# Optimization experiments

Hardware: AMD Instinct MI355X
Metric: run time of the kernel (lower is better)

The kernel has to match this reference:

```python
import jax, jax.numpy as jnp
import numpy as np
from functools import partial

D_MODEL = 768
N_LAYER = 2
VOCAB = 50264  # 50257 padded to multiple of 8
D_STATE = 16
D_INNER = 2 * D_MODEL
DT_RANK = 48
D_CONV = 4
EPS = 1e-5
ZOH_EPS = 1e-7
B, L = 2, 1024


def setup_inputs() -> dict:
    key = jax.random.key(0)
    ks = jax.random.split(key, 16)
    s = 0.02
    inp = {
        'input_ids': jax.random.randint(ks[0], (B, L), 0, VOCAB, dtype=jnp.int32),
        'embedding': jax.random.normal(ks[1], (VOCAB, D_MODEL), jnp.float32) * s,
        'in_w': jax.random.normal(ks[2], (N_LAYER, D_MODEL, 2 * D_INNER), jnp.float32) * s,
        'in_b': jnp.zeros((N_LAYER, 2 * D_INNER), jnp.float32),
        'conv_w': jax.random.normal(ks[3], (N_LAYER, D_INNER, D_CONV), jnp.float32) * s,
        'conv_b': jnp.zeros((N_LAYER, D_INNER), jnp.float32),
        'xproj_w': jax.random.normal(ks[4], (N_LAYER, D_INNER, DT_RANK + 2 * D_STATE), jnp.float32) * s,
        'dt_w': jax.random.normal(ks[5], (N_LAYER, DT_RANK, D_INNER), jnp.float32) * s,
        'dt_b': jnp.zeros((N_LAYER, D_INNER), jnp.float32),
        'A_log': jnp.broadcast_to(jnp.log(jnp.arange(1, D_STATE + 1, dtype=jnp.float32))[None, None, :], (N_LAYER, D_INNER, D_STATE)).copy(),
        'Dp': jnp.ones((N_LAYER, D_INNER), jnp.float32),
        'out_w': jax.random.normal(ks[6], (N_LAYER, D_INNER, D_MODEL), jnp.float32) * s,
        'out_b': jnp.zeros((N_LAYER, D_MODEL), jnp.float32),
        'norm_w': jnp.ones((N_LAYER, D_MODEL), jnp.float32),
        'normf_w': jnp.ones((D_MODEL,), jnp.float32),
    }
    return inp


def rmsnorm(x, w):
    return x * jax.lax.rsqrt(jnp.mean(x * x, axis=-1, keepdims=True) + EPS) * w


def mamba_block(x, in_w, in_b, conv_w, conv_b, xproj_w, dt_w, dt_b, A_log, Dp, out_w, out_b):
    # x: (b, l, d_model)
    xr = x @ in_w + in_b                       # (b, l, 2*d_inner)
    xi, res = jnp.split(xr, 2, axis=-1)        # each (b, l, d_inner)
    # causal depthwise conv1d (torch pads d_conv-1 both sides then truncates to l)
    xc = jnp.transpose(xi, (0, 2, 1))          # (b, d_inner, l)
    xc = jax.lax.conv_general_dilated(
        xc, conv_w[:, None, :], (1,), [(D_CONV - 1, 0)],
        dimension_numbers=('NCH', 'OIH', 'NCH'), feature_group_count=D_INNER)
    xc = xc + conv_b[None, :, None]
    u = jax.nn.silu(jnp.transpose(xc, (0, 2, 1)))  # (b, l, d_inner)
    res = jax.nn.silu(res)
    # generate time-varying SSM params
    dbc = u @ xproj_w                          # (b, l, dt_rank + 2n)
    dt, Bm, Cm = jnp.split(dbc, [DT_RANK, DT_RANK + D_STATE], axis=-1)
    delta = jax.nn.softplus(dt @ dt_w + dt_b)  # (b, l, d_inner)
    A = -jnp.exp(A_log)                        # (d_inner, n)
    # ZOH discretization
    dA = jnp.exp(jnp.einsum('bld,dn->bldn', delta, A))            # (b,l,d_in,n)
    zoh = (dA - 1.0) / (A + ZOH_EPS)                               # (b,l,d_in,n)
    dBu = zoh * Bm[:, :, None, :] * u[..., None]                   # (b,l,d_in,n)
    # selective scan over l
    def step(s, inputs):
        dA_t, dBu_t, C_t = inputs              # (b,d_in,n),(b,d_in,n),(b,n)
        s = dA_t * s + dBu_t
        y = jnp.einsum('bdn,bn->bd', s, C_t)
        return s, y
    s0 = jnp.zeros((u.shape[0], D_INNER, D_STATE), u.dtype)
    _, ys = jax.lax.scan(step, s0, (jnp.moveaxis(dA, 1, 0), jnp.moveaxis(dBu, 1, 0), jnp.moveaxis(Cm, 1, 0)))
    y = jnp.moveaxis(ys, 0, 1) + u * Dp        # (b, l, d_inner)
    y = y * res
    return y @ out_w + out_b


def forward(input_ids, embedding, in_w, in_b, conv_w, conv_b, xproj_w, dt_w, dt_b, A_log, Dp, out_w, out_b, norm_w, normf_w):
    x = embedding[input_ids]                   # (b, l, d_model)
    for i in range(N_LAYER):
        mixed = mamba_block(x, in_w[i], in_b[i], conv_w[i], conv_b[i], xproj_w[i],
                            dt_w[i], dt_b[i], A_log[i], Dp[i], out_w[i], out_b[i])
        x = rmsnorm(mixed + x, norm_w[i])      # ResidualBlock: norm(mixer(x)+x)
    x = rmsnorm(x, normf_w)
    return x @ embedding.T                     # tied lm_head, (b, l, vocab)


def reference(input_ids, embedding, in_w, in_b, conv_w, conv_b, xproj_w, dt_w, dt_b, A_log, Dp, out_w, out_b, norm_w, normf_w):
    return forward(input_ids, embedding, in_w, in_b, conv_w, conv_b, xproj_w,
                   dt_w, dt_b, A_log, Dp, out_w, out_b, norm_w, normf_w)
```

## Files before the change

### kernel.cpp

```cpp
#include <hip/hip_runtime.h>
#include <math.h>
#include <stdint.h>

#define BB 2
#define LL 1024
#define DM 768
#define NL 2
#define VV 50264
#define VPAD 50304
#define DS 16
#define DI 1536
#define DR 48
#define DC 4
#define MM (BB*LL)

#define CH 32
#define NC (LL/CH)
#define CONVL 16

#define KS 8

#define TS 64
#define KT 16

typedef __attribute__((ext_vector_type(8))) short short8;
typedef __attribute__((ext_vector_type(4))) float f32x4;

#define AS3(p) ((__attribute__((address_space(3))) unsigned int*)(unsigned int)(uintptr_t)(p))
#define AS1(p) ((const __attribute__((address_space(1))) unsigned int*)(uintptr_t)(p))

__device__ __forceinline__ unsigned short f2bf(float v) {
    union { float f; unsigned u; } x; x.f = v;
    unsigned r = x.u + 0x7fffu + ((x.u >> 16) & 1u);
    return (unsigned short)(r >> 16);
}
__device__ __forceinline__ float bf2f(unsigned short h) {
    union { unsigned u; float f; } x; x.u = (unsigned)h << 16;
    return x.f;
}

__global__ __launch_bounds__(256) void embed_kernel(
    const int* __restrict__ ids, const float* __restrict__ emb,
    float* __restrict__ x, unsigned short* __restrict__ x16)
{
    int m = blockIdx.x;
    int v = ids[m];
    const float* src = emb + (size_t)v * DM;
    float* dst = x + (size_t)m * DM;
    unsigned short* dst16 = x16 + (size_t)m * DM;
    for (int i = threadIdx.x; i < DM; i += 256) {
        float f = src[i];
        dst[i] = f;
        dst16[i] = f2bf(f);
    }
}

__global__ __launch_bounds__(256) void emb_convert_kernel(
    const float* __restrict__ emb, unsigned short* __restrict__ out)
{
    size_t i8 = (size_t)blockIdx.x * 256 + threadIdx.x;
    size_t row = i8 / 96;
    size_t col8 = (i8 - row * 96) * 8;
    if (row >= VPAD) return;
    ushort4 o0, o1;
    if (row < VV) {
        const float* p = emb + row * DM + col8;
        float4 v0 = *(const float4*)p;
        float4 v1 = *(const float4*)(p + 4);
        o0.x = f2bf(v0.x); o0.y = f2bf(v0.y); o0.z = f2bf(v0.z); o0.w = f2bf(v0.w);
        o1.x = f2bf(v1.x); o1.y = f2bf(v1.y); o1.z = f2bf(v1.z); o1.w = f2bf(v1.w);
    } else {
        o0 = make_ushort4(0, 0, 0, 0);
        o1 = o0;
    }
    unsigned short* op = out + row * DM + col8;
    *(ushort4*)op = o0;
    *(ushort4*)(op + 4) = o1;
}

__global__ __launch_bounds__(256) void transpose_bf16_kernel(
    const float* __restrict__ in, unsigned short* __restrict__ out, int R, int C)
{
    __shared__ float t[32][33];
    int l = blockIdx.z;
    int r0 = blockIdx.y * 32, c0 = blockIdx.x * 32;
    int tx = threadIdx.x & 31, ty = threadIdx.x >> 5;
    const float* ip = in + (size_t)l * R * C;
    unsigned short* op = out + (size_t)l * C * R;
    #pragma unroll
    for (int j = 0; j < 32; j += 8)
        t[ty + j][tx] = ip[(size_t)(r0 + ty + j) * C + c0 + tx];
    __syncthreads();
    #pragma unroll
    for (int j = 0; j < 32; j += 8)
        op[(size_t)(c0 + ty + j) * R + r0 + tx] = f2bf(t[tx][ty + j]);
}

__global__ __launch_bounds__(256) void gemm_mfma_bt(
    const unsigned short* __restrict__ A, const unsigned short* __restrict__ B,
    const float* __restrict__ bias, unsigned short* __restrict__ C16,
    int M, int N, int K, int MT, int NTILES)
{
    int T = MT * NTILES;
    int q = T >> 3, r = T & 7;
    int orig = blockIdx.x;
    int xcd = orig & 7, u = orig >> 3;
    int wg = (xcd < r ? xcd * (q + 1) : r * (q + 1) + (xcd - r) * q) + u;
    int mt = wg % MT, nt = wg / MT;

    __shared__ unsigned short As[3][128 * 32];
    __shared__ unsigned short Bs[3][128 * 32];
    int tid = threadIdx.x;
    int w = tid >> 6, lane = tid & 63;
    int m0 = mt * 128, n0 = nt * 128;

    int rA = lane >> 2;
    int kb = (lane & 3) * 8;
    const unsigned short* gA0 = A + (size_t)(m0 + w * 16 + rA) * K + kb;
    const unsigned short* gA1 = gA0 + (size_t)64 * K;
    const unsigned short* gB0 = B + (size_t)(n0 + w * 16 + rA) * K + kb;
    const unsigned short* gB1 = gB0 + (size_t)64 * K;

    int lr = lane & 15, lk = lane >> 4;
    int wr = (w >> 1) * 64, wc = (w & 1) * 64;

    f32x4 acc[4][4] = {};

#define STAGE(k0, buf) do { \
    __builtin_amdgcn_global_load_lds(AS1(gA0 + (k0)), AS3(&As[buf][(w * 16) * 32]), 16, 0, 0); \
    __builtin_amdgcn_global_load_lds(AS1(gA1 + (k0)), AS3(&As[buf][(64 + w * 16) * 32]), 16, 0, 0); \
    __builtin_amdgcn_global_load_lds(AS1(gB0 + (k0)), AS3(&Bs[buf][(w * 16) * 32]), 16, 0, 0); \
    __builtin_amdgcn_global_load_lds(AS1(gB1 + (k0)), AS3(&Bs[buf][(64 + w * 16) * 32]), 16, 0, 0); \
} while (0)

#define COMPUTE(buf) do { \
    short8 a[4], b[4]; \
    _Pragma("unroll") \
    for (int f = 0; f < 4; ++f) \
        a[f] = *(const short8*)&As[buf][(wr + f * 16 + lr) * 32 + lk * 8]; \
    _Pragma("unroll") \
    for (int f = 0; f < 4; ++f) \
        b[f] = *(const short8*)&Bs[buf][(wc + f * 16 + lr) * 32 + lk * 8]; \
    _Pragma("unroll") \
    for (int i = 0; i < 4; ++i) \
        _Pragma("unroll") \
        for (int j = 0; j < 4; ++j) \
            acc[i][j] = __builtin_amdgcn_mfma_f32_16x16x32_bf16(a[i], b[j], acc[i][j], 0, 0, 0); \
} while (0)

    int nsteps = K / 32;
    STAGE(0, 0);
    STAGE(32, 1);
    asm volatile("s_waitcnt vmcnt(4)" ::: "memory");
    __builtin_amdgcn_s_barrier();
    __builtin_amdgcn_sched_barrier(0);

    for (int t = 0; t < nsteps; ++t) {
        int cur = t % 3;
        if (t + 2 < nsteps)
            STAGE((t + 2) * 32, (t + 2) % 3);
        COMPUTE(cur);
        if (t + 1 < nsteps) {
            if (t + 2 < nsteps)
                asm volatile("s_waitcnt vmcnt(4)" ::: "memory");
            else
                asm volatile("s_waitcnt vmcnt(0)" ::: "memory");
            __builtin_amdgcn_s_barrier();
            __builtin_amdgcn_sched_barrier(0);
        }
    }

#undef STAGE
#undef COMPUTE

    #pragma unroll
    for (int i = 0; i < 4; ++i) {
        int row = m0 + wr + i * 16 + lk * 4;
        #pragma unroll
        for (int j = 0; j < 4; ++j) {
            int col = n0 + wc + j * 16 + lr;
            if (col < N) {
                float bv = bias ? bias[col] : 0.f;
                #pragma unroll
                for (int r2 = 0; r2 < 4; ++r2) {
                    float v = acc[i][j][r2] + bv;
                    C16[(size_t)(row + r2) * N + col] = f2bf(v);
                }
            }
        }
    }
}

__global__ __launch_bounds__(256) void gemm_out_part(
    const unsigned short* __restrict__ A, const unsigned short* __restrict__ B,
    float* __restrict__ part)
{
    const int T = 16 * 6 * 2;
    int q = T >> 3;
    int orig = blockIdx.x;
    int xcd = orig & 7, u = orig >> 3;
    int wg = xcd * q + u;
    int mt = wg % 16;
    int rest = wg / 16;
    int nt = rest % 6, z = rest / 6;

    __shared__ unsigned short As[3][128 * 32];
    __shared__ unsigned short Bs[3][128 * 32];
    int tid = threadIdx.x;
    int w = tid >> 6, lane = tid & 63;
    int m0 = mt * 128, n0 = nt * 128;
    int kh = z * 768;

    int rA = lane >> 2;
    int kb = (lane & 3) * 8;
    const unsigned short* gA0 = A + (size_t)(m0 + w * 16 + rA) * DI + kh + kb;
    const unsigned short* gA1 = gA0 + (size_t)64 * DI;
    const unsigned short* gB0 = B + (size_t)(n0 + w * 16 + rA) * DI + kh + kb;
    const unsigned short* gB1 = gB0 + (size_t)64 * DI;

    int lr = lane & 15, lk = lane >> 4;
    int wr = (w >> 1) * 64, wc = (w & 1) * 64;

    f32x4 acc[4][4] = {};

#define STAGE(k0, buf) do { \
    __builtin_amdgcn_global_load_lds(AS1(gA0 + (k0)), AS3(&As[buf][(w * 16) * 32]), 16, 0, 0); \
    __builtin_amdgcn_global_load_lds(AS1(gA1 + (k0)), AS3(&As[buf][(64 + w * 16) * 32]), 16, 0, 0); \
    __builtin_amdgcn_global_load_lds(AS1(gB0 + (k0)), AS3(&Bs[buf][(w * 16) * 32]), 16, 0, 0); \
    __builtin_amdgcn_global_load_lds(AS1(gB1 + (k0)), AS3(&Bs[buf][(64 + w * 16) * 32]), 16, 0, 0); \
} while (0)

#define COMPUTE(buf) do { \
    short8 a[4], b[4]; \
    _Pragma("unroll") \
    for (int f = 0; f < 4; ++f) \
        a[f] = *(const short8*)&As[buf][(wr + f * 16 + lr) * 32 + lk * 8]; \
    _Pragma("unroll") \
    for (int f = 0; f < 4; ++f) \
        b[f] = *(const short8*)&Bs[buf][(wc + f * 16 + lr) * 32 + lk * 8]; \
    _Pragma("unroll") \
    for (int i = 0; i < 4; ++i) \
        _Pragma("unroll") \
        for (int j = 0; j < 4; ++j) \
            acc[i][j] = __builtin_amdgcn_mfma_f32_16x16x32_bf16(a[i], b[j], acc[i][j], 0, 0, 0); \
} while (0)

    const int nsteps = 768 / 32;
    STAGE(0, 0);
    STAGE(32, 1);
    asm volatile("s_waitcnt vmcnt(4)" ::: "memory");
    __builtin_amdgcn_s_barrier();
    __builtin_amdgcn_sched_barrier(0);

    for (int t = 0; t < nsteps; ++t) {
        int cur = t % 3;
        if (t + 2 < nsteps)
            STAGE((t + 2) * 32, (t + 2) % 3);
        COMPUTE(cur);
        if (t + 1 < nsteps) {
            if (t + 2 < nsteps)
                asm volatile("s_waitcnt vmcnt(4)" ::: "memory");
            else
                asm volatile("s_waitcnt vmcnt(0)" ::: "memory");
            __builtin_amdgcn_s_barrier();
            __builtin_amdgcn_sched_barrier(0);
        }
    }

#undef STAGE
#undef COMPUTE

    float* op = part + (size_t)z * MM * DM;
    #pragma unroll
    for (int i = 0; i < 4; ++i) {
        int row = m0 + wr + i * 16 + lk * 4;
        #pragma unroll
        for (int j = 0; j < 4; ++j) {
            int col = n0 + wc + j * 16 + lr;
            #pragma unroll
            for (int r2 = 0; r2 < 4; ++r2)
                op[(size_t)(row + r2) * DM + col] = acc[i][j][r2];
        }
    }
}

__global__ __launch_bounds__(512) void gemm_logits(
    const unsigned short* __restrict__ A, const unsigned short* __restrict__ B,
    float* __restrict__ C, int M, int N, int K, int MT, int NTILES)
{
    int T = MT * NTILES;
    int q = T >> 3, r = T & 7;
    int orig = blockIdx.x;
    int xcd = orig & 7, u = orig >> 3;
    int wg = (xcd < r ? xcd * (q + 1) : r * (q + 1) + (xcd - r) * q) + u;
    int mt = wg % MT, nt = wg / MT;

    __shared__ unsigned short As[3][256 * 32];
    __shared__ unsigned short Bs[3][128 * 32];
    int tid = threadIdx.x;
    int w = tid >> 6, lane = tid & 63;
    int wm = w >> 1, wn = w & 1;
    int m0 = mt * 256, n0 = nt * 128;

    int srow = tid >> 2;
    int schunk = (tid & 3) ^ ((srow & 3) ^ ((srow >> 2) & 3));
    const unsigned short* gA0 = A + (size_t)(m0 + srow) * K + schunk * 8;
    const unsigned short* gA1 = gA0 + (size_t)128 * K;
    const unsigned short* gB0 = B + (size_t)(n0 + srow) * K + schunk * 8;

    int lr = lane & 15, lk = lane >> 4;
    int rc = (lk ^ ((lr & 3) ^ ((lr >> 2) & 3))) * 8;

    f32x4 acc[4][4] = {};

#define STAGE_A(k0, buf) do { \
    __builtin_amdgcn_global_load_lds(AS1(gA0 + (k0)), AS3(&As[buf][(w * 16) * 32]), 16, 0, 0); \
    __builtin_amdgcn_global_load_lds(AS1(gA1 + (k0)), AS3(&As[buf][(128 + w * 16) * 32]), 16, 0, 0); \
} while (0)
#define STAGE_B(k0, buf) do { \
    __builtin_amdgcn_global_load_lds(AS1(gB0 + (k0)), AS3(&Bs[buf][(w * 16) * 32]), 16, 0, 0); \
} while (0)

    int nsteps = K / 32;

    STAGE_A(0, 0); STAGE_B(0, 0);
    STAGE_A(32, 1); STAGE_B(32, 1);
    asm volatile("s_waitcnt vmcnt(3)" ::: "memory");
    __builtin_amdgcn_s_barrier();
    __builtin_amdgcn_sched_barrier(0);

    for (int t = 0; t < nsteps; ++t) {
        int s = t % 3;
        int sn = (t + 2) % 3;
        bool stage2 = (t + 2) < nsteps;
        short8 av[2], bv[4];

        #pragma unroll
        for (int f = 0; f < 2; ++f)
            av[f] = *(const short8*)&As[s][(wm * 64 + f * 16 + lr) * 32 + rc];
        #pragma unroll
        for (int f = 0; f < 4; ++f)
            bv[f] = *(const short8*)&Bs[s][(wn * 64 + f * 16 + lr) * 32 + rc];
        if (stage2) STAGE_A((t + 2) * 32, sn);
        __builtin_amdgcn_s_barrier();
        asm volatile("s_waitcnt lgkmcnt(0)" ::: "memory");
        __builtin_amdgcn_sched_barrier(0);
        __builtin_amdgcn_s_setprio(1);
        #pragma unroll
        for (int i = 0; i < 2; ++i)
            #pragma unroll
            for (int j = 0; j < 4; ++j)
                acc[i][j] = __builtin_amdgcn_mfma_f32_16x16x32_bf16(av[i], bv[j], acc[i][j], 0, 0, 0);
        __builtin_amdgcn_s_setprio(0);
        __builtin_amdgcn_s_barrier();

        #pragma unroll
        for (int f = 0; f < 2; ++f)
            av[f] = *(const short8*)&As[s][(wm * 64 + (2 + f) * 16 + lr) * 32 + rc];
        if (stage2) STAGE_B((t + 2) * 32, sn);
        __builtin_amdgcn_s_barrier();
        asm volatile("s_waitcnt lgkmcnt(0)" ::: "memory");
        __builtin_amdgcn_sched_barrier(0);
        __builtin_amdgcn_s_setprio(1);
        #pragma unroll
        for (int i = 0; i < 2; ++i)
            #pragma unroll
            for (int j = 0; j < 4; ++j)
                acc[2 + i][j] = __builtin_amdgcn_mfma_f32_16x16x32_bf16(av[i], bv[j], acc[2 + i][j], 0, 0, 0);
        __builtin_amdgcn_s_setprio(0);

        if (t + 1 < nsteps) {
            if (stage2)
                asm volatile("s_waitcnt vmcnt(3)" ::: "memory");
            else
                asm volatile("s_waitcnt vmcnt(0)" ::: "memory");
            __builtin_amdgcn_s_barrier();
            __builtin_amdgcn_sched_barrier(0);
        }
    }

#undef STAGE_A
#undef STAGE_B

    #pragma unroll
    for (int i = 0; i < 4; ++i) {
        int row = m0 + wm * 64 + i * 16 + lk * 4;
        #pragma unroll
        for (int j = 0; j < 4; ++j) {
            int col = n0 + wn * 64 + j * 16 + lr;
            if (col < N) {
                #pragma unroll
                for (int r2 = 0; r2 < 4; ++r2)
                    C[(size_t)(row + r2) * N + col] = acc[i][j][r2];
            }
        }
    }
}

__global__ __launch_bounds__(256) void dt_kernel(
    const float* __restrict__ A, const float* __restrict__ Bm,
    const float* __restrict__ bias, unsigned short* __restrict__ C16,
    int M, int N, int K, int lda)
{
    __shared__ float As[KT][TS + 4];
    __shared__ float Bs[KT][TS + 4];
    int tid = threadIdx.x;
    int tx = tid & 15, ty = tid >> 4;
    int m0 = blockIdx.y * TS;
    int n0 = blockIdx.x * TS;
    float acc[4][4] = {};

    for (int k0 = 0; k0 < K; k0 += KT) {
        {
            int i = tid >> 2;
            int k4 = (tid & 3) * 4;
            float4 v = *(const float4*)(A + (size_t)(m0 + i) * lda + k0 + k4);
            As[k4 + 0][i] = v.x; As[k4 + 1][i] = v.y;
            As[k4 + 2][i] = v.z; As[k4 + 3][i] = v.w;
        }
        {
            int k = tid >> 4;
            int j4 = (tid & 15) * 4;
            float4 v = *(const float4*)(Bm + (size_t)(k0 + k) * N + n0 + j4);
            Bs[k][j4 + 0] = v.x; Bs[k][j4 + 1] = v.y;
            Bs[k][j4 + 2] = v.z; Bs[k][j4 + 3] = v.w;
        }
        __syncthreads();
        #pragma unroll
        for (int k = 0; k < KT; ++k) {
            float a[4], b[4];
            #pragma unroll
            for (int q2 = 0; q2 < 4; ++q2) a[q2] = As[k][ty * 4 + q2];
            #pragma unroll
            for (int q2 = 0; q2 < 4; ++q2) b[q2] = Bs[k][tx * 4 + q2];
            #pragma unroll
            for (int i = 0; i < 4; ++i)
                #pragma unroll
                for (int j = 0; j < 4; ++j)
                    acc[i][j] = fmaf(a[i], b[j], acc[i][j]);
        }
        __syncthreads();
    }

    #pragma unroll
    for (int i = 0; i < 4; ++i) {
        int m = m0 + ty * 4 + i;
        #pragma unroll
        for (int j = 0; j < 4; ++j) {
            int n = n0 + tx * 4 + j;
            float v = acc[i][j] + bias[n];
            v = fmaxf(v, 0.f) + log1pf(expf(-fabsf(v)));
            C16[(size_t)m * N + n] = f2bf(v);
        }
    }
}

__global__ __launch_bounds__(256) void xproj_part_kernel(
    const unsigned short* __restrict__ A, const float* __restrict__ Bm,
    float* __restrict__ part)
{
    __shared__ float As[KT][TS + 4];
    __shared__ float Bs[KT][TS + 4];
    int tid = threadIdx.x;
    int tx = tid & 15, ty = tid >> 4;
    int m0 = blockIdx.y * TS;
    int n0 = blockIdx.x * TS;
    int kbeg = blockIdx.z * (DI / KS);
    const int N = 80;
    float acc[4][4] = {};

    for (int k0 = kbeg; k0 < kbeg + DI / KS; k0 += KT) {
        {
            int i = tid >> 2;
            int k4 = (tid & 3) * 4;
            ushort4 hv = *(const ushort4*)(A + (size_t)(m0 + i) * DI + k0 + k4);
            As[k4 + 0][i] = bf2f(hv.x); As[k4 + 1][i] = bf2f(hv.y);
            As[k4 + 2][i] = bf2f(hv.z); As[k4 + 3][i] = bf2f(hv.w);
        }
        {
            int k = tid >> 4;
            int j4 = (tid & 15) * 4;
            int n = n0 + j4;
            const float* p = Bm + (size_t)(k0 + k) * N + n;
            float4 v;
            if (n + 3 < N) {
                v = *(const float4*)p;
            } else {
                v.x = (n + 0 < N) ? p[0] : 0.f;
                v.y = (n + 1 < N) ? p[1] : 0.f;
                v.z = (n + 2 < N) ? p[2] : 0.f;
                v.w = (n + 3 < N) ? p[3] : 0.f;
            }
            Bs[k][j4 + 0] = v.x; Bs[k][j4 + 1] = v.y;
            Bs[k][j4 + 2] = v.z; Bs[k][j4 + 3] = v.w;
        }
        __syncthreads();
        #pragma unroll
        for (int k = 0; k < KT; ++k) {
            float a[4], b[4];
            #pragma unroll
            for (int q2 = 0; q2 < 4; ++q2) a[q2] = As[k][ty * 4 + q2];
            #pragma unroll
            for (int q2 = 0; q2 < 4; ++q2) b[q2] = Bs[k][tx * 4 + q2];
            #pragma unroll
            for (int i = 0; i < 4; ++i)
                #pragma unroll
                for (int j = 0; j < 4; ++j)
                    acc[i][j] = fmaf(a[i], b[j], acc[i][j]);
        }
        __syncthreads();
    }

    float* op = part + (size_t)blockIdx.z * MM * 80;
    #pragma unroll
    for (int i = 0; i < 4; ++i) {
        int m = m0 + ty * 4 + i;
        #pragma unroll
        for (int j = 0; j < 4; ++j) {
            int n = n0 + tx * 4 + j;
            if (n < 80) op[(size_t)m * 80 + n] = acc[i][j];
        }
    }
}

__global__ __launch_bounds__(256) void xproj_reduce_kernel(
    const float* __restrict__ part, float* __restrict__ dbc)
{
    int i = blockIdx.x * 256 + threadIdx.x;
    if (i >= MM * 80) return;
    float s = 0.f;
    #pragma unroll
    for (int z = 0; z < KS; ++z) s += part[(size_t)z * MM * 80 + i];
    dbc[i] = s;
}

__global__ __launch_bounds__(256) void conv_silu_kernel(
    const unsigned short* __restrict__ xr, const float* __restrict__ cw,
    const float* __restrict__ cb, unsigned short* __restrict__ u)
{
    int d = blockIdx.x * 256 + threadIdx.x;
    int l0 = blockIdx.y * CONVL;
    int b = blockIdx.z;
    const float4 wv = *(const float4*)(cw + (size_t)d * DC);
    float bias = cb[d];
    const unsigned short* xp = xr + ((size_t)(b * LL + l0)) * (2 * DI) + d;
    unsigned short* up = u + ((size_t)(b * LL + l0)) * DI + d;
    const ptrdiff_t RS = 2 * DI;
    float xm3 = (l0 >= 3) ? bf2f(xp[-3 * RS]) : 0.f;
    float xm2 = (l0 >= 2) ? bf2f(xp[-2 * RS]) : 0.f;
    float xm1 = (l0 >= 1) ? bf2f(xp[-1 * RS]) : 0.f;
    #pragma unroll
    for (int l = 0; l < CONVL; ++l) {
        float xc = bf2f(xp[(ptrdiff_t)l * RS]);
        float acc = bias;
        acc = fmaf(wv.x, xm3, acc);
        acc = fmaf(wv.y, xm2, acc);
        acc = fmaf(wv.z, xm1, acc);
        acc = fmaf(wv.w, xc, acc);
        float s = acc / (1.f + expf(-acc));
        up[(size_t)l * DI] = f2bf(s);
        xm3 = xm2; xm2 = xm1; xm1 = xc;
    }
}

__global__ __launch_bounds__(256) void scan_reduce_kernel(
    const unsigned short* __restrict__ delta, const unsigned short* __restrict__ u,
    const float* __restrict__ dbc, const float* __restrict__ A_log,
    float* __restrict__ P, float* __restrict__ Q)
{
    int d = blockIdx.x * 256 + threadIdx.x;
    int c = blockIdx.y;
    int b = blockIdx.z;

    float Av[DS], invA[DS];
    {
        const float4* ap = (const float4*)(A_log + (size_t)d * DS);
        #pragma unroll
        for (int n4 = 0; n4 < 4; ++n4) {
            float4 a = ap[n4];
            Av[n4 * 4 + 0] = -expf(a.x); Av[n4 * 4 + 1] = -expf(a.y);
            Av[n4 * 4 + 2] = -expf(a.z); Av[n4 * 4 + 3] = -expf(a.w);
        }
        #pragma unroll
        for (int n = 0; n < DS; ++n) invA[n] = 1.f / (Av[n] + 1e-7f);
    }

    float p[DS], s[DS];
    #pragma unroll
    for (int n = 0; n < DS; ++n) { p[n] = 1.f; s[n] = 0.f; }

    const unsigned short* dp = delta + ((size_t)b * LL + c * CH) * DI + d;
    const unsigned short* up = u     + ((size_t)b * LL + c * CH) * DI + d;
    const float* bb = dbc + ((size_t)b * LL + c * CH) * 80 + DR;

    for (int l = 0; l < CH; ++l) {
        float dlt = bf2f(dp[(size_t)l * DI]);
        float uv  = bf2f(up[(size_t)l * DI]);
        float Bv[DS];
        {
            const float4* bp4 = (const float4*)(bb + (size_t)l * 80);
            #pragma unroll
            for (int n4 = 0; n4 < 4; ++n4) {
                float4 v = bp4[n4];
                Bv[n4 * 4 + 0] = v.x; Bv[n4 * 4 + 1] = v.y;
                Bv[n4 * 4 + 2] = v.z; Bv[n4 * 4 + 3] = v.w;
            }
        }
        #pragma unroll
        for (int n = 0; n < DS; ++n) {
            float dA = expf(dlt * Av[n]);
            float dBu = (dA - 1.f) * invA[n] * Bv[n] * uv;
            p[n] *= dA;
            s[n] = fmaf(dA, s[n], dBu);
        }
    }

    float* Pp = P + (((size_t)b * NC + c) * DI + d) * DS;
    float* Qp = Q + (((size_t)b * NC + c) * DI + d) * DS;
    #pragma unroll
    for (int n4 = 0; n4 < 4; ++n4) {
        ((float4*)Pp)[n4] = make_float4(p[n4 * 4 + 0], p[n4 * 4 + 1], p[n4 * 4 + 2], p[n4 * 4 + 3]);
        ((float4*)Qp)[n4] = make_float4(s[n4 * 4 + 0], s[n4 * 4 + 1], s[n4 * 4 + 2], s[n4 * 4 + 3]);
    }
}

__global__ __launch_bounds__(256) void scan_combine_kernel(
    const float* __restrict__ P, const float* __restrict__ Q, float* __restrict__ Sinit)
{
    int t = blockIdx.x * 256 + threadIdx.x;
    int b = t / (DI * DS);
    int dn = t - b * (DI * DS);
    float s = 0.f;
    for (int c = 0; c < NC; ++c) {
        size_t idx = ((size_t)b * NC + c) * (DI * DS) + dn;
        Sinit[idx] = s;
        s = fmaf(P[idx], s, Q[idx]);
    }
}

__global__ __launch_bounds__(256) void scan_apply_kernel(
    const unsigned short* __restrict__ delta, const unsigned short* __restrict__ u,
    const float* __restrict__ dbc, const unsigned short* __restrict__ xr,
    const float* __restrict__ A_log, const float* __restrict__ Dp,
    const float* __restrict__ Sinit, unsigned short* __restrict__ y16)
{
    int d = blockIdx.x * 256 + threadIdx.x;
    int c = blockIdx.y;
    int b = blockIdx.z;

    float Av[DS], invA[DS];
    {
        const float4* ap = (const float4*)(A_log + (size_t)d * DS);
        #pragma unroll
        for (int n4 = 0; n4 < 4; ++n4) {
            float4 a = ap[n4];
            Av[n4 * 4 + 0] = -expf(a.x); Av[n4 * 4 + 1] = -expf(a.y);
            Av[n4 * 4 + 2] = -expf(a.z); Av[n4 * 4 + 3] = -expf(a.w);
        }
        #pragma unroll
        for (int n = 0; n < DS; ++n) invA[n] = 1.f / (Av[n] + 1e-7f);
    }
    float Dv = Dp[d];

    float s[DS];
    {
        const float4* Sp = (const float4*)(Sinit + (((size_t)b * NC + c) * DI + d) * DS);
        #pragma unroll
        for (int n4 = 0; n4 < 4; ++n4) {
            float4 sw = Sp[n4];
            s[n4 * 4 + 0] = sw.x; s[n4 * 4 + 1] = sw.y;
            s[n4 * 4 + 2] = sw.z; s[n4 * 4 + 3] = sw.w;
        }
    }

    const unsigned short* dp = delta + ((size_t)b * LL + c * CH) * DI + d;
    const unsigned short* up = u     + ((size_t)b * LL + c * CH) * DI + d;
    const unsigned short* xp = xr    + ((size_t)b * LL + c * CH) * (2 * DI) + DI + d;
    const float* bb = dbc + ((size_t)b * LL + c * CH) * 80 + DR;
    unsigned short* yp = y16 + ((size_t)b * LL + c * CH) * DI + d;

    for (int l = 0; l < CH; ++l) {
        float dlt = bf2f(dp[(size_t)l * DI]);
        float uv  = bf2f(up[(size_t)l * DI]);
        float rv  = bf2f(xp[(size_t)l * (2 * DI)]);
        float Bv[DS], Cv[DS];
        {
            const float4* bp4 = (const float4*)(bb + (size_t)l * 80);
            #pragma unroll
            for (int n4 = 0; n4 < 4; ++n4) {
                float4 v = bp4[n4];
                Bv[n4 * 4 + 0] = v.x; Bv[n4 * 4 + 1] = v.y;
                Bv[n4 * 4 + 2] = v.z; Bv[n4 * 4 + 3] = v.w;
            }
            #pragma unroll
            for (int n4 = 0; n4 < 4; ++n4) {
                float4 v = bp4[4 + n4];
                Cv[n4 * 4 + 0] = v.x; Cv[n4 * 4 + 1] = v.y;
                Cv[n4 * 4 + 2] = v.z; Cv[n4 * 4 + 3] = v.w;
            }
        }
        float pv = 0.f;
        #pragma unroll
        for (int n = 0; n < DS; ++n) {
            float dA = expf(dlt * Av[n]);
            float dBu = (dA - 1.f) * invA[n] * Bv[n] * uv;
            s[n] = fmaf(dA, s[n], dBu);
            pv = fmaf(s[n], Cv[n], pv);
        }
        float res = rv / (1.f + expf(-rv));
        yp[(size_t)l * DI] = f2bf((pv + uv * Dv) * res);
    }
}

__global__ __launch_bounds__(256) void rmsnorm_kernel(
    const float* __restrict__ in, const float* __restrict__ w,
    float* __restrict__ outf, unsigned short* __restrict__ outb)
{
    int m = blockIdx.x;
    const float* row = in + (size_t)m * DM;
    float ss = 0.f;
    for (int i = threadIdx.x; i < DM; i += 256) { float v = row[i]; ss = fmaf(v, v, ss); }
    #pragma unroll
    for (int off = 32; off > 0; off >>= 1) ss += __shfl_down(ss, off);
    __shared__ float sred[4];
    __shared__ float sscale;
    int wid = threadIdx.x >> 6;
    if ((threadIdx.x & 63) == 0) sred[wid] = ss;
    __syncthreads();
    if (threadIdx.x == 0) {
        float tot = sred[0] + sred[1] + sred[2] + sred[3];
        sscale = 1.f / sqrtf(tot / (float)DM + 1e-5f);
    }
    __syncthreads();
    float sc = sscale;
    for (int i = threadIdx.x; i < DM; i += 256) {
        float v = row[i] * sc * w[i];
        if (outf) outf[(size_t)m * DM + i] = v;
        if (outb) outb[(size_t)m * DM + i] = f2bf(v);
    }
}

__global__ __launch_bounds__(256) void rmsnorm_fuse_kernel(
    const float* __restrict__ p0, const float* __restrict__ p1,
    const float* __restrict__ ob, const float* __restrict__ w,
    float* __restrict__ x, unsigned short* __restrict__ x16)
{
    int m = blockIdx.x;
    int tid = threadIdx.x;
    float v0, v1, v2;
    float ss = 0.f;
    {
        size_t base = (size_t)m * DM;
        v0 = p0[base + tid] + p1[base + tid] + x[base + tid] + ob[tid];
        v1 = p0[base + tid + 256] + p1[base + tid + 256] + x[base + tid + 256] + ob[tid + 256];
        v2 = p0[base + tid + 512] + p1[base + tid + 512] + x[base + tid + 512] + ob[tid + 512];
        ss = fmaf(v0, v0, fmaf(v1, v1, v2 * v2));
    }
    #pragma unroll
    for (int off = 32; off > 0; off >>= 1) ss += __shfl_down(ss, off);
    __shared__ float sred[4];
    __shared__ float sscale;
    int wid = tid >> 6;
    if ((tid & 63) == 0) sred[wid] = ss;
    __syncthreads();
    if (tid == 0) {
        float tot = sred[0] + sred[1] + sred[2] + sred[3];
        sscale = 1.f / sqrtf(tot / (float)DM + 1e-5f);
    }
    __syncthreads();
    float sc = sscale;
    size_t base = (size_t)m * DM;
    float o0 = v0 * sc * w[tid];
    float o1 = v1 * sc * w[tid + 256];
    float o2 = v2 * sc * w[tid + 512];
    x[base + tid] = o0;         x16[base + tid] = f2bf(o0);
    x[base + tid + 256] = o1;   x16[base + tid + 256] = f2bf(o1);
    x[base + tid + 512] = o2;   x16[base + tid + 512] = f2bf(o2);
}

extern "C" void kernel_launch(void* const* d_in, const int* in_sizes, int n_in,
                              void* d_out, int out_size, void* d_ws, size_t ws_size,
                              hipStream_t stream)
{
    const int*   ids      = (const int*)  d_in[0];
    const float* emb      = (const float*)d_in[1];
    const float* in_w     = (const float*)d_in[2];
    const float* in_b     = (const float*)d_in[3];
    const float* conv_w   = (const float*)d_in[4];
    const float* conv_b   = (const float*)d_in[5];
    const float* xproj_w  = (const float*)d_in[6];
    const float* dt_w     = (const float*)d_in[7];
    const float* dt_b     = (const float*)d_in[8];
    const float* A_log    = (const float*)d_in[9];
    const float* Dp       = (const float*)d_in[10];
    const float* out_w    = (const float*)d_in[11];
    const float* out_b    = (const float*)d_in[12];
    const float* norm_w   = (const float*)d_in[13];
    const float* normf_w  = (const float*)d_in[14];
    float* out = (float*)d_out;

    char* wsp = (char*)d_ws;
    auto alloc = [&](size_t bytes) {
        char* p = wsp;
        wsp += (bytes + 255) & ~(size_t)255;
        return p;
    };
    float* x     = (float*)alloc((size_t)MM * DM * 4);
    unsigned short* xr    = (unsigned short*)alloc((size_t)MM * 2 * DI * 2);
    unsigned short* ub    = (unsigned short*)alloc((size_t)MM * DI * 2);
    float* dbc   = (float*)alloc((size_t)MM * 80 * 4);
    float* part  = (float*)alloc((size_t)KS * MM * 80 * 4);
    unsigned short* delta = (unsigned short*)alloc((size_t)MM * DI * 2);
    float* oprt  = (float*)alloc((size_t)2 * MM * DM * 4);
    float* Pbuf  = (float*)alloc((size_t)BB * NC * DI * DS * 4);
    float* Qbuf  = (float*)alloc((size_t)BB * NC * DI * DS * 4);
    float* Sbuf  = (float*)alloc((size_t)BB * NC * DI * DS * 4);
    unsigned short* x16     = (unsigned short*)alloc((size_t)MM * DM * 2);
    unsigned short* y16     = (unsigned short*)alloc((size_t)MM * DI * 2);
    unsigned short* emb16   = (unsigned short*)alloc((size_t)VPAD * DM * 2);
    unsigned short* in_wT   = (unsigned short*)alloc((size_t)NL * 2 * DI * DM * 2);
    unsigned short* out_wT  = (unsigned short*)alloc((size_t)NL * DM * DI * 2);

    emb_convert_kernel<<<((size_t)VPAD * (DM / 8) + 255) / 256, 256, 0, stream>>>(emb, emb16);
    transpose_bf16_kernel<<<dim3(2 * DI / 32, DM / 32, NL), 256, 0, stream>>>(
        in_w, in_wT, DM, 2 * DI);
    transpose_bf16_kernel<<<dim3(DM / 32, DI / 32, NL), 256, 0, stream>>>(
        out_w, out_wT, DI, DM);

    embed_kernel<<<MM, 256, 0, stream>>>(ids, emb, x, x16);

    for (int layer = 0; layer < NL; ++layer) {
        const float* lb_in  = in_b    + (size_t)layer * 2 * DI;
        const float* lcw    = conv_w  + (size_t)layer * DI * DC;
        const float* lcb    = conv_b  + (size_t)layer * DI;
        const float* lxw    = xproj_w + (size_t)layer * DI * (DR + 2 * DS);
        const float* ldtw   = dt_w    + (size_t)layer * DR * DI;
        const float* ldtb   = dt_b    + (size_t)layer * DI;
        const float* lAlog  = A_log   + (size_t)layer * DI * DS;
        const float* lDp    = Dp      + (size_t)layer * DI;
        const float* lob    = out_b   + (size_t)layer * DM;
        const float* lnw    = norm_w  + (size_t)layer * DM;
        const unsigned short* lw_inT = in_wT  + (size_t)layer * 2 * DI * DM;
        const unsigned short* lw_outT= out_wT + (size_t)layer * DM * DI;

        gemm_mfma_bt<<<16 * 24, 256, 0, stream>>>(
            x16, lw_inT, lb_in, xr, MM, 2 * DI, DM, 16, 24);

        conv_silu_kernel<<<dim3(DI / 256, LL / CONVL, BB), 256, 0, stream>>>(xr, lcw, lcb, ub);

        xproj_part_kernel<<<dim3(2, MM / TS, KS), 256, 0, stream>>>(ub, lxw, part);
        xproj_reduce_kernel<<<(MM * 80 + 255) / 256, 256, 0, stream>>>(part, dbc);

        dt_kernel<<<dim3(DI / TS, MM / TS), 256, 0, stream>>>(
            dbc, ldtw, ldtb, delta, MM, DI, DR, DR + 2 * DS);

        scan_reduce_kernel<<<dim3(DI / 256, NC, BB), 256, 0, stream>>>(
            delta, ub, dbc, lAlog, Pbuf, Qbuf);
        scan_combine_kernel<<<(BB * DI * DS) / 256, 256, 0, stream>>>(Pbuf, Qbuf, Sbuf);
        scan_apply_kernel<<<dim3(DI / 256, NC, BB), 256, 0, stream>>>(
            delta, ub, dbc, xr, lAlog, lDp, Sbuf, y16);

        gemm_out_part<<<192, 256, 0, stream>>>(y16, lw_outT, oprt);

        rmsnorm_fuse_kernel<<<MM, 256, 0, stream>>>(
            oprt, oprt + (size_t)MM * DM, lob, lnw, x, x16);
    }

    rmsnorm_kernel<<<MM, 256, 0, stream>>>(x, normf_w, nullptr, x16);

    gemm_logits<<<8 * (VPAD / 128), 512, 0, stream>>>(
        x16, emb16, out, MM, VV, DM, 8, VPAD / 128);
}
```

Before: 730.4 us.

## Move x_proj and dt_proj GEMMs onto bf16 MFMA kernels

Replaces the scalar fp32 tiled x_proj and dt_proj GEMMs with bf16 MFMA kernels that stage tiles through LDS using direct global-to-LDS loads. The x_proj and dt_proj weights are transposed and padded to bf16 (128 and 64 wide) once at setup, and the split-K reduce now also emits a padded bf16 copy of the dt-rank columns for the dt GEMM. This cuts FMA-bound compute in two small per-layer GEMMs, at the cost of bf16 rounding of the dt-rank inputs and weights and two extra conversion launches.

```diff
diff --git a/kernel.cpp b/kernel.cpp
--- a/kernel.cpp
+++ b/kernel.cpp
@@ -19,9 +19,6 @@
 #define CONVL 16
 
 #define KS 8
-
-#define TS 64
-#define KT 16
 
 typedef __attribute__((ext_vector_type(8))) short short8;
 typedef __attribute__((ext_vector_type(4))) float f32x4;
@@ -96,6 +93,48 @@
         op[(size_t)(c0 + ty + j) * R + r0 + tx] = f2bf(t[tx][ty + j]);
 }
 
+__global__ __launch_bounds__(256) void xprojw_convert_kernel(
+    const float* __restrict__ in, unsigned short* __restrict__ out)
+{
+    __shared__ float t[32][33];
+    int l = blockIdx.z;
+    int r0 = blockIdx.y * 32;
+    int c0 = blockIdx.x * 32;
+    int tx = threadIdx.x & 31, ty = threadIdx.x >> 5;
+    const float* ip = in + (size_t)l * DI * 80;
+    unsigned short* op = out + (size_t)l * 128 * DI;
+    #pragma unroll
+    for (int j = 0; j < 32; j += 8) {
+        int c = c0 + tx;
+        t[ty + j][tx] = (c < 80) ? ip[(size_t)(r0 + ty + j) * 80 + c] : 0.f;
+    }
+    __syncthreads();
+    #pragma unroll
+    for (int j = 0; j < 32; j += 8)
+        op[(size_t)(c0 + ty + j) * DI + r0 + tx] = f2bf(t[tx][ty + j]);
+}
+
+__global__ __launch_bounds__(256) void dtw_convert_kernel(
+    const float* __restrict__ in, unsigned short* __restrict__ out)
+{
+    __shared__ float t[32][33];
+    int l = blockIdx.z;
+    int r0 = blockIdx.y * 32;
+    int c0 = blockIdx.x * 32;
+    int tx = threadIdx.x & 31, ty = threadIdx.x >> 5;
+    const float* ip = in + (size_t)l * DR * DI;
+    unsigned short* op = out + (size_t)l * DI * 64;
+    #pragma unroll
+    for (int j = 0; j < 32; j += 8) {
+        int r = r0 + ty + j;
+        t[ty + j][tx] = (r < DR) ? ip[(size_t)r * DI + c0 + tx] : 0.f;
+    }
+    __syncthreads();
+    #pragma unroll
+    for (int j = 0; j < 32; j += 8)
+        op[(size_t)(c0 + ty + j) * 64 + r0 + tx] = f2bf(t[tx][ty + j]);
+}
+
 __global__ __launch_bounds__(256) void gemm_mfma_bt(
     const unsigned short* __restrict__ A, const unsigned short* __restrict__ B,
     const float* __restrict__ bias, unsigned short* __restrict__ C16,
@@ -284,6 +323,188 @@
     }
 }
 
+__global__ __launch_bounds__(256) void xproj_mfma_part(
+    const unsigned short* __restrict__ A, const unsigned short* __restrict__ B,
+    float* __restrict__ part)
+{
+    int mt = blockIdx.x % 16;
+    int z  = blockIdx.x / 16;
+
+    __shared__ unsigned short As[3][128 * 32];
+    __shared__ unsigned short Bs[3][128 * 32];
+    int tid = threadIdx.x;
+    int w = tid >> 6, lane = tid & 63;
+    int m0 = mt * 128;
+    int kh = z * (DI / KS);
+
+    int rA = lane >> 2;
+    int kb = (lane & 3) * 8;
+    const unsigned short* gA0 = A + (size_t)(m0 + w * 16 + rA) * DI + kh + kb;
+    const unsigned short* gA1 = gA0 + (size_t)64 * DI;
+    const unsigned short* gB0 = B + (size_t)(w * 16 + rA) * DI + kh + kb;
+    const unsigned short* gB1 = gB0 + (size_t)64 * DI;
+
+    int lr = lane & 15, lk = lane >> 4;
+    int wr = (w >> 1) * 64, wc = (w & 1) * 64;
+
+    f32x4 acc[4][4] = {};
+
+#define STAGE(k0, buf) do { \
+    __builtin_amdgcn_global_load_lds(AS1(gA0 + (k0)), AS3(&As[buf][(w * 16) * 32]), 16, 0, 0); \
+    __builtin_amdgcn_global_load_lds(AS1(gA1 + (k0)), AS3(&As[buf][(64 + w * 16) * 32]), 16, 0, 0); \
+    __builtin_amdgcn_global_load_lds(AS1(gB0 + (k0)), AS3(&Bs[buf][(w * 16) * 32]), 16, 0, 0); \
+    __builtin_amdgcn_global_load_lds(AS1(gB1 + (k0)), AS3(&Bs[buf][(64 + w * 16) * 32]), 16, 0, 0); \
+} while (0)
+
+#define COMPUTE(buf) do { \
+    short8 a[4], b[4]; \
+    _Pragma("unroll") \
+    for (int f = 0; f < 4; ++f) \
+        a[f] = *(const short8*)&As[buf][(wr + f * 16 + lr) * 32 + lk * 8]; \
+    _Pragma("unroll") \
+    for (int f = 0; f < 4; ++f) \
+        b[f] = *(const short8*)&Bs[buf][(wc + f * 16 + lr) * 32 + lk * 8]; \
+    _Pragma("unroll") \
+    for (int i = 0; i < 4; ++i) \
+        _Pragma("unroll") \
+        for (int j = 0; j < 4; ++j) \
+            acc[i][j] = __builtin_amdgcn_mfma_f32_16x16x32_bf16(a[i], b[j], acc[i][j], 0, 0, 0); \
+} while (0)
+
+    const int nsteps = (DI / KS) / 32;
+    STAGE(0, 0);
+    STAGE(32, 1);
+    asm volatile("s_waitcnt vmcnt(4)" ::: "memory");
+    __builtin_amdgcn_s_barrier();
+    __builtin_amdgcn_sched_barrier(0);
+
+    for (int t = 0; t < nsteps; ++t) {
+        int cur = t % 3;
+        if (t + 2 < nsteps)
+            STAGE((t + 2) * 32, (t + 2) % 3);
+        COMPUTE(cur);
+        if (t + 1 < nsteps) {
+            if (t + 2 < nsteps)
+                asm volatile("s_waitcnt vmcnt(4)" ::: "memory");
+            else
+                asm volatile("s_waitcnt vmcnt(0)" ::: "memory");
+            __builtin_amdgcn_s_barrier();
+            __builtin_amdgcn_sched_barrier(0);
+        }
+    }
+
+#undef STAGE
+#undef COMPUTE
+
+    float* op = part + (size_t)z * MM * 80;
+    #pragma unroll
+    for (int i = 0; i < 4; ++i) {
+        int row = m0 + wr + i * 16 + lk * 4;
+        #pragma unroll
+        for (int j = 0; j < 4; ++j) {
+            int col = wc + j * 16 + lr;
+            if (col < 80) {
+                #pragma unroll
+                for (int r2 = 0; r2 < 4; ++r2)
+                    op[(size_t)(row + r2) * 80 + col] = acc[i][j][r2];
+            }
+        }
+    }
+}
+
+__global__ __launch_bounds__(256) void xproj_reduce_kernel(
+    const float* __restrict__ part, float* __restrict__ dbc,
+    unsigned short* __restrict__ dbc48)
+{
+    int i = blockIdx.x * 256 + threadIdx.x;
+    if (i >= MM * 80) return;
+    float s = 0.f;
+    #pragma unroll
+    for (int z = 0; z < KS; ++z) s += part[(size_t)z * MM * 80 + i];
+    dbc[i] = s;
+    int m = i / 80, col = i - m * 80;
+    if (col < DR) dbc48[(size_t)m * 64 + col] = f2bf(s);
+    else if (col < 64) dbc48[(size_t)m * 64 + col] = 0;
+}
+
+__global__ __launch_bounds__(256) void dt_mfma(
+    const unsigned short* __restrict__ A, const unsigned short* __restrict__ B,
+    const float* __restrict__ bias, unsigned short* __restrict__ C16)
+{
+    int mt = blockIdx.x % 16;
+    int nt = blockIdx.x / 16;
+
+    __shared__ unsigned short As[2][128 * 32];
+    __shared__ unsigned short Bs[2][128 * 32];
+    int tid = threadIdx.x;
+    int w = tid >> 6, lane = tid & 63;
+    int m0 = mt * 128, n0 = nt * 128;
+
+    int rA = lane >> 2;
+    int kb = (lane & 3) * 8;
+    const unsigned short* gA0 = A + (size_t)(m0 + w * 16 + rA) * 64 + kb;
+    const unsigned short* gA1 = gA0 + (size_t)64 * 64;
+    const unsigned short* gB0 = B + (size_t)(n0 + w * 16 + rA) * 64 + kb;
+    const unsigned short* gB1 = gB0 + (size_t)64 * 64;
+
+    int lr = lane & 15, lk = lane >> 4;
+    int wr = (w >> 1) * 64, wc = (w & 1) * 64;
+
+    f32x4 acc[4][4] = {};
+
+#define STAGE(k0, buf) do { \
+    __builtin_amdgcn_global_load_lds(AS1(gA0 + (k0)), AS3(&As[buf][(w * 16) * 32]), 16, 0, 0); \
+    __builtin_amdgcn_global_load_lds(AS1(gA1 + (k0)), AS3(&As[buf][(64 + w * 16) * 32]), 16, 0, 0); \
+    __builtin_amdgcn_global_load_lds(AS1(gB0 + (k0)), AS3(&Bs[buf][(w * 16) * 32]), 16, 0, 0); \
+    __builtin_amdgcn_global_load_lds(AS1(gB1 + (k0)), AS3(&Bs[buf][(64 + w * 16) * 32]), 16, 0, 0); \
+} while (0)
+
+#define COMPUTE(buf) do { \
+    short8 a[4], b[4]; \
+    _Pragma("unroll") \
+    for (int f = 0; f < 4; ++f) \
+        a[f] = *(const short8*)&As[buf][(wr + f * 16 + lr) * 32 + lk * 8]; \
+    _Pragma("unroll") \
+    for (int f = 0; f < 4; ++f) \
+        b[f] = *(const short8*)&Bs[buf][(wc + f * 16 + lr) * 32 + lk * 8]; \
+    _Pragma("unroll") \
+    for (int i = 0; i < 4; ++i) \
+        _Pragma("unroll") \
+        for (int j = 0; j < 4; ++j) \
+            acc[i][j] = __builtin_amdgcn_mfma_f32_16x16x32_bf16(a[i], b[j], acc[i][j], 0, 0, 0); \
+} while (0)
+
+    STAGE(0, 0);
+    STAGE(32, 1);
+    asm volatile("s_waitcnt vmcnt(4)" ::: "memory");
+    __builtin_amdgcn_s_barrier();
+    __builtin_amdgcn_sched_barrier(0);
+    COMPUTE(0);
+    asm volatile("s_waitcnt vmcnt(0)" ::: "memory");
+    __builtin_amdgcn_s_barrier();
+    __builtin_amdgcn_sched_barrier(0);
+    COMPUTE(1);
+
+#undef STAGE
+#undef COMPUTE
+
+    #pragma unroll
+    for (int i = 0; i < 4; ++i) {
+        int row = m0 + wr + i * 16 + lk * 4;
+        #pragma unroll
+        for (int j = 0; j < 4; ++j) {
+            int col = n0 + wc + j * 16 + lr;
+            float bv = bias[col];
+            #pragma unroll
+            for (int r2 = 0; r2 < 4; ++r2) {
+                float v = acc[i][j][r2] + bv;
+                v = fmaxf(v, 0.f) + log1pf(expf(-fabsf(v)));
+                C16[(size_t)(row + r2) * DI + col] = f2bf(v);
+            }
+        }
+    }
+}
+
 __global__ __launch_bounds__(512) void gemm_logits(
     const unsigned short* __restrict__ A, const unsigned short* __restrict__ B,
     float* __restrict__ C, int M, int N, int K, int MT, int NTILES)
@@ -395,143 +616,6 @@
             }
         }
     }
-}
-
-__global__ __launch_bounds__(256) void dt_kernel(
-    const float* __restrict__ A, const float* __restrict__ Bm,
-    const float* __restrict__ bias, unsigned short* __restrict__ C16,
-    int M, int N, int K, int lda)
-{
-    __shared__ float As[KT][TS + 4];
-    __shared__ float Bs[KT][TS + 4];
-    int tid = threadIdx.x;
-    int tx = tid & 15, ty = tid >> 4;
-    int m0 = blockIdx.y * TS;
-    int n0 = blockIdx.x * TS;
-    float acc[4][4] = {};
-
-    for (int k0 = 0; k0 < K; k0 += KT) {
-        {
-            int i = tid >> 2;
-            int k4 = (tid & 3) * 4;
-            float4 v = *(const float4*)(A + (size_t)(m0 + i) * lda + k0 + k4);
-            As[k4 + 0][i] = v.x; As[k4 + 1][i] = v.y;
-            As[k4 + 2][i] = v.z; As[k4 + 3][i] = v.w;
-        }
-        {
-            int k = tid >> 4;
-            int j4 = (tid & 15) * 4;
-            float4 v = *(const float4*)(Bm + (size_t)(k0 + k) * N + n0 + j4);
-            Bs[k][j4 + 0] = v.x; Bs[k][j4 + 1] = v.y;
-            Bs[k][j4 + 2] = v.z; Bs[k][j4 + 3] = v.w;
-        }
-        __syncthreads();
-        #pragma unroll
-        for (int k = 0; k < KT; ++k) {
-            float a[4], b[4];
-            #pragma unroll
-            for (int q2 = 0; q2 < 4; ++q2) a[q2] = As[k][ty * 4 + q2];
-            #pragma unroll
-            for (int q2 = 0; q2 < 4; ++q2) b[q2] = Bs[k][tx * 4 + q2];
-            #pragma unroll
-            for (int i = 0; i < 4; ++i)
-                #pragma unroll
-                for (int j = 0; j < 4; ++j)
-                    acc[i][j] = fmaf(a[i], b[j], acc[i][j]);
-        }
-        __syncthreads();
-    }
-
-    #pragma unroll
-    for (int i = 0; i < 4; ++i) {
-        int m = m0 + ty * 4 + i;
-        #pragma unroll
-        for (int j = 0; j < 4; ++j) {
-            int n = n0 + tx * 4 + j;
-            float v = acc[i][j] + bias[n];
-            v = fmaxf(v, 0.f) + log1pf(expf(-fabsf(v)));
-            C16[(size_t)m * N + n] = f2bf(v);
-        }
-    }
-}
-
-__global__ __launch_bounds__(256) void xproj_part_kernel(
-    const unsigned short* __restrict__ A, const float* __restrict__ Bm,
-    float* __restrict__ part)
-{
-    __shared__ float As[KT][TS + 4];
-    __shared__ float Bs[KT][TS + 4];
-    int tid = threadIdx.x;
-    int tx = tid & 15, ty = tid >> 4;
-    int m0 = blockIdx.y * TS;
-    int n0 = blockIdx.x * TS;
-    int kbeg = blockIdx.z * (DI / KS);
-    const int N = 80;
-    float acc[4][4] = {};
-
-    for (int k0 = kbeg; k0 < kbeg + DI / KS; k0 += KT) {
-        {
-            int i = tid >> 2;
-            int k4 = (tid & 3) * 4;
-            ushort4 hv = *(const ushort4*)(A + (size_t)(m0 + i) * DI + k0 + k4);
-            As[k4 + 0][i] = bf2f(hv.x); As[k4 + 1][i] = bf2f(hv.y);
-            As[k4 + 2][i] = bf2f(hv.z); As[k4 + 3][i] = bf2f(hv.w);
-        }
-        {
-            int k = tid >> 4;
-            int j4 = (tid & 15) * 4;
-            int n = n0 + j4;
-            const float* p = Bm + (size_t)(k0 + k) * N + n;
-            float4 v;
-            if (n + 3 < N) {
-                v = *(const float4*)p;
-            } else {
-                v.x = (n + 0 < N) ? p[0] : 0.f;
-                v.y = (n + 1 < N) ? p[1] : 0.f;
-                v.z = (n + 2 < N) ? p[2] : 0.f;
-                v.w = (n + 3 < N) ? p[3] : 0.f;
-            }
-            Bs[k][j4 + 0] = v.x; Bs[k][j4 + 1] = v.y;
-            Bs[k][j4 + 2] = v.z; Bs[k][j4 + 3] = v.w;
-        }
-        __syncthreads();
-        #pragma unroll
-        for (int k = 0; k < KT; ++k) {
-            float a[4], b[4];
-            #pragma unroll
-            for (int q2 = 0; q2 < 4; ++q2) a[q2] = As[k][ty * 4 + q2];
-            #pragma unroll
-            for (int q2 = 0; q2 < 4; ++q2) b[q2] = Bs[k][tx * 4 + q2];
-            #pragma unroll
-            for (int i = 0; i < 4; ++i)
-                #pragma unroll
-                for (int j = 0; j < 4; ++j)
-                    acc[i][j] = fmaf(a[i], b[j], acc[i][j]);
-        }
-        __syncthreads();
-    }
-
-    float* op = part + (size_t)blockIdx.z * MM * 80;
-    #pragma unroll
-    for (int i = 0; i < 4; ++i) {
-        int m = m0 + ty * 4 + i;
-        #pragma unroll
-        for (int j = 0; j < 4; ++j) {
-            int n = n0 + tx * 4 + j;
-            if (n < 80) op[(size_t)m * 80 + n] = acc[i][j];
-        }
-    }
-}
-
-__global__ __launch_bounds__(256) void xproj_reduce_kernel(
-    const float* __restrict__ part, float* __restrict__ dbc)
-{
-    int i = blockIdx.x * 256 + threadIdx.x;
-    if (i >= MM * 80) return;
-    float s = 0.f;
-    #pragma unroll
-    for (int z = 0; z < KS; ++z) s += part[(size_t)z * MM * 80 + i];
-    dbc[i] = s;
 }
 
 __global__ __launch_bounds__(256) void conv_silu_kernel(
@@ -809,6 +893,7 @@
     unsigned short* xr    = (unsigned short*)alloc((size_t)MM * 2 * DI * 2);
     unsigned short* ub    = (unsigned short*)alloc((size_t)MM * DI * 2);
     float* dbc   = (float*)alloc((size_t)MM * 80 * 4);
+    unsigned short* dbc48 = (unsigned short*)alloc((size_t)MM * 64 * 2);
     float* part  = (float*)alloc((size_t)KS * MM * 80 * 4);
     unsigned short* delta = (unsigned short*)alloc((size_t)MM * DI * 2);
     float* oprt  = (float*)alloc((size_t)2 * MM * DM * 4);
@@ -820,12 +905,16 @@
     unsigned short* emb16   = (unsigned short*)alloc((size_t)VPAD * DM * 2);
     unsigned short* in_wT   = (unsigned short*)alloc((size_t)NL * 2 * DI * DM * 2);
     unsigned short* out_wT  = (unsigned short*)alloc((size_t)NL * DM * DI * 2);
+    unsigned short* xprojT  = (unsigned short*)alloc((size_t)NL * 128 * DI * 2);
+    unsigned short* dtwT    = (unsigned short*)alloc((size_t)NL * DI * 64 * 2);
 
     emb_convert_kernel<<<((size_t)VPAD * (DM / 8) + 255) / 256, 256, 0, stream>>>(emb, emb16);
     transpose_bf16_kernel<<<dim3(2 * DI / 32, DM / 32, NL), 256, 0, stream>>>(
         in_w, in_wT, DM, 2 * DI);
     transpose_bf16_kernel<<<dim3(DM / 32, DI / 32, NL), 256, 0, stream>>>(
         out_w, out_wT, DI, DM);
+    xprojw_convert_kernel<<<dim3(4, DI / 32, NL), 256, 0, stream>>>(xproj_w, xprojT);
+    dtw_convert_kernel<<<dim3(DI / 32, 2, NL), 256, 0, stream>>>(dt_w, dtwT);
 
     embed_kernel<<<MM, 256, 0, stream>>>(ids, emb, x, x16);
 
@@ -833,8 +922,6 @@
         const float* lb_in  = in_b    + (size_t)layer * 2 * DI;
         const float* lcw    = conv_w  + (size_t)layer * DI * DC;
         const float* lcb    = conv_b  + (size_t)layer * DI;
-        const float* lxw    = xproj_w + (size_t)layer * DI * (DR + 2 * DS);
-        const float* ldtw   = dt_w    + (size_t)layer * DR * DI;
         const float* ldtb   = dt_b    + (size_t)layer * DI;
         const float* lAlog  = A_log   + (size_t)layer * DI * DS;
         const float* lDp    = Dp      + (size_t)layer * DI;
@@ -842,17 +929,18 @@
         const float* lnw    = norm_w  + (size_t)layer * DM;
         const unsigned short* lw_inT = in_wT  + (size_t)layer * 2 * DI * DM;
         const unsigned short* lw_outT= out_wT + (size_t)layer * DM * DI;
+        const unsigned short* lxT    = xprojT + (size_t)layer * 128 * DI;
+        const unsigned short* ldtT   = dtwT   + (size_t)layer * DI * 64;
 
         gemm_mfma_bt<<<16 * 24, 256, 0, stream>>>(
             x16, lw_inT, lb_in, xr, MM, 2 * DI, DM, 16, 24);
 
         conv_silu_kernel<<<dim3(DI / 256, LL / CONVL, BB), 256, 0, stream>>>(xr, lcw, lcb, ub);
 
-        xproj_part_kernel<<<dim3(2, MM / TS, KS), 256, 0, stream>>>(ub, lxw, part);
-        xproj_reduce_kernel<<<(MM * 80 + 255) / 256, 256, 0, stream>>>(part, dbc);
-
-        dt_kernel<<<dim3(DI / TS, MM / TS), 256, 0, stream>>>(
-            dbc, ldtw, ldtb, delta, MM, DI, DR, DR + 2 * DS);
+        xproj_mfma_part<<<16 * KS, 256, 0, stream>>>(ub, lxT, part);
+        xproj_reduce_kernel<<<(MM * 80 + 255) / 256, 256, 0, stream>>>(part, dbc, dbc48);
+
+        dt_mfma<<<16 * 12, 256, 0, stream>>>(dbc48, ldtT, ldtb, delta);
 
         scan_reduce_kernel<<<dim3(DI / 256, NC, BB), 256, 0, stream>>>(
             delta, ub, dbc, lAlog, Pbuf, Qbuf);
```

Measured after the change: 863.5 us. 1.18x slower.
